# Kernel optimization log

Hardware: AMD Instinct MI355X
Metric: run time of the kernel (lower is better)

The kernel has to match this reference:

```python
import jax, jax.numpy as jnp
import numpy as np

B, L, U = 64, 512, 7          # batch, seq_len, enc_in
H = 128                        # hidden_dim
LAYERS = 2                     # num LSTM layers
PRED = 96                      # pred_len
EPS = 1e-5


def setup_inputs() -> dict:
    key = jax.random.key(0)
    ks = jax.random.split(key, 9)
    s = 0.05  # small param scale for numerical sanity
    return {
        "x": jax.random.normal(ks[0], (B, L, U), dtype=jnp.float32),
        "emb_W": jax.random.normal(ks[1], (H, 1), dtype=jnp.float32) * s,
        "emb_b": jax.random.normal(ks[2], (H,), dtype=jnp.float32) * s,
        "Wih": jax.random.normal(ks[3], (LAYERS, 4 * H, H), dtype=jnp.float32) * s,
        "Whh": jax.random.normal(ks[4], (LAYERS, 4 * H, H), dtype=jnp.float32) * s,
        "bih": jax.random.normal(ks[5], (LAYERS, 4 * H), dtype=jnp.float32) * s,
        "bhh": jax.random.normal(ks[6], (LAYERS, 4 * H), dtype=jnp.float32) * s,
        "fc_W": jax.random.normal(ks[7], (PRED, H), dtype=jnp.float32) * s,
        "fc_b": jax.random.normal(ks[8], (PRED,), dtype=jnp.float32) * s,
    }


def _lstm_layer(x, Wih, Whh, bih, bhh):
    """PyTorch-semantics single LSTM layer. x: [N, L, H_in] -> [N, L, H]."""
    N = x.shape[0]
    Hh = Whh.shape[1]
    # precompute input projections for all timesteps: [N, L, 4H]
    xp = jnp.einsum('nli,gi->nlg', x, Wih) + bih + bhh
    xp = jnp.swapaxes(xp, 0, 1)  # [L, N, 4H] for scan over time

    def step(carry, xt):
        h, c = carry
        gates = xt + h @ Whh.T           # [N, 4H]
        i, f, g, o = jnp.split(gates, 4, axis=-1)  # torch gate order i,f,g,o
        i = jax.nn.sigmoid(i)
        f = jax.nn.sigmoid(f)
        g = jnp.tanh(g)
        o = jax.nn.sigmoid(o)
        c = f * c + i * g
        h = o * jnp.tanh(c)
        return (h, c), h

    h0 = jnp.zeros((N, Hh), x.dtype)
    (_, _), hs = jax.lax.scan(step, (h0, h0), xp)
    return jnp.swapaxes(hs, 0, 1)  # [N, L, H]


def reference(x, emb_W, emb_b, Wih, Whh, bih, bhh, fc_W, fc_b):
    Bn, Ln, Un = x.shape
    # per-channel instance norm over time (stats detached in original)
    means = jax.lax.stop_gradient(jnp.mean(x, axis=1, keepdims=True))          # [B,1,U]
    stdev = jax.lax.stop_gradient(jnp.sqrt(jnp.var(x, axis=1, keepdims=True) + EPS))
    xn = (x - means) / stdev
    # NOTE: original does a raw row-major reshape (no channel permute); replicate exactly.
    xs = xn.reshape(Bn * Un, Ln, 1)                                            # [B*U, L, 1]
    h = xs @ emb_W.T + emb_b                                                   # [B*U, L, H]
    for l in range(Wih.shape[0]):
        h = _lstm_layer(h, Wih[l], Whh[l], bih[l], bhh[l])
    out = h[:, -1, :] @ fc_W.T + fc_b                                          # [B*U, PRED]
    out = out.reshape(Bn, -1, Un)                                              # [B, PRED, U]
    return out * stdev + means
```

## Files before the change

kernel.cpp:

```cpp
#include <hip/hip_runtime.h>
#include <stdint.h>

typedef short bf16x8 __attribute__((ext_vector_type(8)));
typedef float f32x4  __attribute__((ext_vector_type(4)));

#define HH 128
#define NN 448
#define PREDN 96

#define OFF_MEAN 0
#define OFF_STD  448
#define OFF_A    896
#define OFF_B0   1408
#define OFF_B1   1920
#define OFF_H1   2432
#define OFF_XSB  59776
#define OFF_WPK  174464

#define L2E  1.442695041f
#define L2E2 2.885390082f

#define ROWB 592
#define BUFB 9472

__device__ __forceinline__ float bflo(uint32_t w){ union{uint32_t u; float f;} v; v.u = w<<16; return v.f; }
__device__ __forceinline__ float bfhi(uint32_t w){ union{uint32_t u; float f;} v; v.u = w & 0xffff0000u; return v.f; }

static __device__ __forceinline__ uint32_t packbf2(float a, float b){
    union { float f; uint32_t u; } ua, ub; ua.f = a; ub.f = b;
    uint32_t x = ua.u, y = ub.u;
    uint32_t lo = (x + 0x7fffu + ((x>>16)&1u)) >> 16;
    uint32_t hi = (y + 0x7fffu + ((y>>16)&1u)) >> 16;
    return (lo & 0xffffu) | (hi<<16);
}
static __device__ __forceinline__ uint16_t bfr(float f){
    union { float f; uint32_t u; } v; v.f = f;
    return (uint16_t)((v.u + 0x7fffu + ((v.u>>16)&1u)) >> 16);
}

#if __has_builtin(__builtin_amdgcn_exp2f)
#define EXP2(x) __builtin_amdgcn_exp2f(x)
#else
#define EXP2(x) __expf(0.69314718056f*(x))
#endif
#if __has_builtin(__builtin_amdgcn_rcpf)
#define RCPF(x) __builtin_amdgcn_rcpf(x)
#else
#define RCPF(x) (1.0f/(x))
#endif

__device__ __forceinline__ float sig2(float x){ return RCPF(1.f + EXP2(-x)); }
__device__ __forceinline__ float tanh2(float xs){ return fmaf(-2.f, RCPF(EXP2(xs) + 1.f), 1.f); }

__global__ void stats_k(const float* __restrict__ x, float* __restrict__ ws){
    int bu = blockIdx.x;
    int b = bu / 7, u = bu % 7;
    int i = threadIdx.x;
    const float* p = x + b*3584 + u;
    float s = 0.f, q = 0.f;
    #pragma unroll
    for (int m=0;m<8;m++){ float v = p[(i + 64*m)*7]; s += v; q += v*v; }
    for (int o=32;o>0;o>>=1){ s += __shfl_down(s,o); q += __shfl_down(q,o); }
    if (i==0){
        float mean = s * (1.f/512.f);
        float var  = q * (1.f/512.f) - mean*mean;
        ws[OFF_MEAN + bu] = mean;
        ws[OFF_STD  + bu] = sqrtf(var + 1e-5f);
    }
}

__global__ void norm_k(const float* __restrict__ x, float* __restrict__ ws){
    int i = blockIdx.x*256 + threadIdx.x;
    int b = i / 3584, u = i % 7;
    float m = ws[OFF_MEAN + b*7 + u];
    float sd = ws[OFF_STD + b*7 + u];
    float v = (x[i] - m) / sd;
    int np = i >> 9, tp = i & 511;
    uint16_t* xb = (uint16_t*)(ws + OFF_XSB);
    xb[(np>>4)*8192 + tp*16 + (np&15)] = (uint16_t)(packbf2(v, 0.f) & 0xffffu);
}

__global__ void prep_k(const float* __restrict__ Wih, const float* __restrict__ embW,
                       const float* __restrict__ embb, const float* __restrict__ bih,
                       const float* __restrict__ bhh, float* __restrict__ ws){
    int g = threadIdx.x;
    const float* wr = Wih + g*HH;
    float a = 0.f, bb = 0.f;
    #pragma unroll 4
    for (int k=0;k<HH;k++){ a += wr[k]*embW[k]; bb += wr[k]*embb[k]; }
    ws[OFF_A  + g] = a;
    ws[OFF_B0 + g] = bb + bih[g] + bhh[g];
    ws[OFF_B1 + g] = bih[512 + g] + bhh[512 + g];
}

__global__ void prep2_k(const float* __restrict__ Whh, const float* __restrict__ Wih,
                        float* __restrict__ ws){
    int idx = blockIdx.x*256 + threadIdx.x;
    int lane = idx & 63;
    int sg = idx >> 6;
    int wvmt = sg / 13, slot = sg % 13;
    int gp  = wvmt*16 + (lane&15);
    int type = gp & 3, unit = gp >> 2;
    int row = type*128 + unit;
    float S = (type==2) ? L2E2 : L2E;
    uint4 r;
    if (slot == 4){
        r.x = r.y = r.z = r.w = 0u;
        if ((lane>>4) == 0) r.x = packbf2(ws[OFF_A+row]*S, ws[OFF_B0+row]*S);
    } else {
        const float* src; int kk;
        if (slot < 4)      { src = Whh + row*128;         kk = slot;   }
        else if (slot < 9) { src = Wih + 65536 + row*128; kk = slot-5; }
        else               { src = Whh + 65536 + row*128; kk = slot-9; }
        int k0 = kk*32 + (lane>>4)*8;
        r.x = packbf2(src[k0]*S,   src[k0+1]*S);
        r.y = packbf2(src[k0+2]*S, src[k0+3]*S);
        r.z = packbf2(src[k0+4]*S, src[k0+5]*S);
        r.w = packbf2(src[k0+6]*S, src[k0+7]*S);
    }
    ((uint4*)(ws + OFF_WPK))[sg*64 + lane] = r;
}

union FragU { bf16x8 v; uint4 q; };

__device__ __forceinline__ f32x4 mm(bf16x8 a, bf16x8 b, f32x4 c){
    return __builtin_amdgcn_mfma_f32_16x16x32_bf16(a, b, c, 0, 0, 0);
}
#define LD(p) (*(const bf16x8*)(p))

__global__ __launch_bounds__(512, 2) void lstm_core(float* __restrict__ ws)
{
    __shared__ uint16_t xsT[8192];
    __shared__ __align__(16) uint16_t hbuf[BUFB];

    const int tid = threadIdx.x;
    const int wv = tid>>6, l = tid&63;
    const int r   = l & 15;
    const int q16 = (l>>4)*16;
    const int bx = blockIdx.x, n0 = bx*16;
    char* hb = (char*)hbuf;

    const uint16_t* xb = (const uint16_t*)(ws + OFF_XSB) + bx*8192;
    for (int i=tid;i<8192;i+=512) xsT[i] = xb[i];
    for (int i=tid;i<BUFB;i+=512) hbuf[i] = 0;
    __syncthreads();
    if (tid < 32){
        int bsel = tid>>4, rr = tid&15;
        *(uint16_t*)(hb + bsel*BUFB + rr*ROWB + 514) = 0x3F80;
    }
    if (tid < 16){
        *(uint16_t*)(hb + tid*ROWB + 512) = xsT[tid];
    }

    bf16x8 wL0[4][5], wI1[4][4], wH1[4][4];
    uint32_t b1pk[4][2];
    const uint4* wpk = (const uint4*)(ws + OFF_WPK);
    #pragma unroll
    for (int mt=0;mt<4;++mt){
        int base = ((wv*4+mt)*13)*64 + l;
        #pragma unroll
        for (int kk=0;kk<5;kk++){ FragU u; u.q = wpk[base + kk*64];     wL0[mt][kk]=u.v; }
        #pragma unroll
        for (int kk=0;kk<4;kk++){ FragU u; u.q = wpk[base + (5+kk)*64]; wI1[mt][kk]=u.v; }
        #pragma unroll
        for (int kk=0;kk<4;kk++){ FragU u; u.q = wpk[base + (9+kk)*64]; wH1[mt][kk]=u.v; }
        int uu = (wv*4+mt)*4 + (l>>4);
        b1pk[mt][0] = packbf2(ws[OFF_B1+uu]*L2E,      ws[OFF_B1+128+uu]*L2E);
        b1pk[mt][1] = packbf2(ws[OFF_B1+256+uu]*L2E2, ws[OFF_B1+384+uu]*L2E);
    }

    float c0[4]={0,0,0,0}, c1[4]={0,0,0,0};
    const int rbase = r*ROWB + q16;
    const int wbase = r*ROWB + wv*32 + 2*(l>>4);

    __syncthreads();

    for (int t=0;t<512;++t){
        const int co = (t&1)*BUFB;
        const int no = BUFB - co;
        const char* pc = hb + co + rbase;
        char* pw = hb + no + wbase;

        bf16x8 f0 = LD(pc+0), f1 = LD(pc+64), f2 = LD(pc+128), f3 = LD(pc+192);
        f32x4 b0={0,0,0,0}, b1={0,0,0,0}, b2={0,0,0,0}, b3={0,0,0,0};
        __builtin_amdgcn_s_setprio(1);
        b0=mm(wI1[0][0],f0,b0); b1=mm(wI1[1][0],f0,b1); b2=mm(wI1[2][0],f0,b2); b3=mm(wI1[3][0],f0,b3);
        b0=mm(wI1[0][1],f1,b0); b1=mm(wI1[1][1],f1,b1); b2=mm(wI1[2][1],f1,b2); b3=mm(wI1[3][1],f1,b3);
        b0=mm(wI1[0][2],f2,b0); b1=mm(wI1[1][2],f2,b1); b2=mm(wI1[2][2],f2,b2); b3=mm(wI1[3][2],f2,b3);
        b0=mm(wI1[0][3],f3,b0); b1=mm(wI1[1][3],f3,b1); b2=mm(wI1[2][3],f3,b2); b3=mm(wI1[3][3],f3,b3);
        bf16x8 fa = LD(pc+512);
        f32x4 a0={0,0,0,0}, a1={0,0,0,0}, a2={0,0,0,0}, a3={0,0,0,0};
        a0=mm(wL0[0][0],f0,a0); a1=mm(wL0[1][0],f0,a1); a2=mm(wL0[2][0],f0,a2); a3=mm(wL0[3][0],f0,a3);
        a0=mm(wL0[0][1],f1,a0); a1=mm(wL0[1][1],f1,a1); a2=mm(wL0[2][1],f1,a2); a3=mm(wL0[3][1],f1,a3);
        a0=mm(wL0[0][2],f2,a0); a1=mm(wL0[1][2],f2,a1); a2=mm(wL0[2][2],f2,a2); a3=mm(wL0[3][2],f2,a3);
        a0=mm(wL0[0][3],f3,a0); a1=mm(wL0[1][3],f3,a1); a2=mm(wL0[2][3],f3,a2); a3=mm(wL0[3][3],f3,a3);
        a0=mm(wL0[0][4],fa,a0); a1=mm(wL0[1][4],fa,a1); a2=mm(wL0[2][4],fa,a2); a3=mm(wL0[3][4],fa,a3);
        __builtin_amdgcn_s_setprio(0);

        #pragma unroll
        for (int mt=0;mt<4;++mt){
            f32x4 a = (mt==0)?a0:(mt==1)?a1:(mt==2)?a2:a3;
            float i_ = sig2(a[0]);
            float f_ = sig2(a[1]);
            float g_ = tanh2(a[2]);
            float o_ = sig2(a[3]);
            float cn = fmaf(f_, c0[mt], i_*g_);
            c0[mt] = cn;
            float h = o_ * tanh2(cn*L2E2);
            *(uint16_t*)(pw + 8*mt) = bfr(h);
        }

        __builtin_amdgcn_sched_barrier(0);
        bf16x8 v0 = LD(pc+256), v1 = LD(pc+320), v2 = LD(pc+384), v3 = LD(pc+448);
        __builtin_amdgcn_s_setprio(1);
        b0=mm(wH1[0][0],v0,b0); b1=mm(wH1[1][0],v0,b1); b2=mm(wH1[2][0],v0,b2); b3=mm(wH1[3][0],v0,b3);
        b0=mm(wH1[0][1],v1,b0); b1=mm(wH1[1][1],v1,b1); b2=mm(wH1[2][1],v1,b2); b3=mm(wH1[3][1],v1,b3);
        b0=mm(wH1[0][2],v2,b0); b1=mm(wH1[1][2],v2,b1); b2=mm(wH1[2][2],v2,b2); b3=mm(wH1[3][2],v2,b3);
        b0=mm(wH1[0][3],v3,b0); b1=mm(wH1[1][3],v3,b1); b2=mm(wH1[2][3],v3,b2); b3=mm(wH1[3][3],v3,b3);
        __builtin_amdgcn_s_setprio(0);

        if (t){
            #pragma unroll
            for (int mt=0;mt<4;++mt){
                f32x4 a = (mt==0)?b0:(mt==1)?b1:(mt==2)?b2:b3;
                float i_ = sig2(a[0] + bflo(b1pk[mt][0]));
                float f_ = sig2(a[1] + bfhi(b1pk[mt][0]));
                float g_ = tanh2(a[2] + bflo(b1pk[mt][1]));
                float o_ = sig2(a[3] + bfhi(b1pk[mt][1]));
                float cn = fmaf(f_, c1[mt], i_*g_);
                c1[mt] = cn;
                float h = o_ * tanh2(cn*L2E2);
                *(uint16_t*)(pw + 256 + 8*mt) = bfr(h);
            }
        }
        if (wv==0 && l<16){
            *(uint16_t*)(hb + no + l*ROWB + 512) = xsT[((t+1)&511)*16 + l];
        }
        __syncthreads();
    }

    {
        const char* pc = hb + rbase;
        bf16x8 f0 = LD(pc+0),   f1 = LD(pc+64),  f2 = LD(pc+128), f3 = LD(pc+192);
        bf16x8 v0 = LD(pc+256), v1 = LD(pc+320), v2 = LD(pc+384), v3 = LD(pc+448);
        f32x4 b0={0,0,0,0}, b1={0,0,0,0}, b2={0,0,0,0}, b3={0,0,0,0};
        b0=mm(wI1[0][0],f0,b0); b1=mm(wI1[1][0],f0,b1); b2=mm(wI1[2][0],f0,b2); b3=mm(wI1[3][0],f0,b3);
        b0=mm(wI1[0][1],f1,b0); b1=mm(wI1[1][1],f1,b1); b2=mm(wI1[2][1],f1,b2); b3=mm(wI1[3][1],f1,b3);
        b0=mm(wI1[0][2],f2,b0); b1=mm(wI1[1][2],f2,b1); b2=mm(wI1[2][2],f2,b2); b3=mm(wI1[3][2],f2,b3);
        b0=mm(wI1[0][3],f3,b0); b1=mm(wI1[1][3],f3,b1); b2=mm(wI1[2][3],f3,b2); b3=mm(wI1[3][3],f3,b3);
        b0=mm(wH1[0][0],v0,b0); b1=mm(wH1[1][0],v0,b1); b2=mm(wH1[2][0],v0,b2); b3=mm(wH1[3][0],v0,b3);
        b0=mm(wH1[0][1],v1,b0); b1=mm(wH1[1][1],v1,b1); b2=mm(wH1[2][1],v1,b2); b3=mm(wH1[3][1],v1,b3);
        b0=mm(wH1[0][2],v2,b0); b1=mm(wH1[1][2],v2,b1); b2=mm(wH1[2][2],v2,b2); b3=mm(wH1[3][2],v2,b3);
        b0=mm(wH1[0][3],v3,b0); b1=mm(wH1[1][3],v3,b1); b2=mm(wH1[2][3],v3,b2); b3=mm(wH1[3][3],v3,b3);
        #pragma unroll
        for (int mt=0;mt<4;++mt){
            f32x4 a = (mt==0)?b0:(mt==1)?b1:(mt==2)?b2:b3;
            float i_ = sig2(a[0] + bflo(b1pk[mt][0]));
            float f_ = sig2(a[1] + bfhi(b1pk[mt][0]));
            float g_ = tanh2(a[2] + bflo(b1pk[mt][1]));
            float o_ = sig2(a[3] + bfhi(b1pk[mt][1]));
            float cn = fmaf(f_, c1[mt], i_*g_);
            float h = o_ * tanh2(cn*L2E2);
            ws[OFF_H1 + (n0+r)*128 + (wv*16 + mt*4 + (l>>4))] = h;
        }
    }
}

__global__ void out_k(const float* __restrict__ fcW, const float* __restrict__ fcb,
                      const float* __restrict__ ws, float* __restrict__ out){
    __shared__ float hl[128];
    int n = blockIdx.x, tid = threadIdx.x;
    hl[tid] = ws[OFF_H1 + n*128 + tid];
    __syncthreads();
    if (tid < PREDN){
        float acc = fcb[tid];
        const float* wr = fcW + tid*128;
        #pragma unroll 4
        for (int k=0;k<128;k++) acc += wr[k]*hl[k];
        int idx = n*PREDN + tid;
        int b = idx / 672, u = idx % 7;
        out[idx] = acc * ws[OFF_STD + b*7 + u] + ws[OFF_MEAN + b*7 + u];
    }
}

extern "C" void kernel_launch(void* const* d_in, const int* in_sizes, int n_in,
                              void* d_out, int out_size, void* d_ws, size_t ws_size,
                              hipStream_t stream)
{
    const float* x    = (const float*)d_in[0];
    const float* embW = (const float*)d_in[1];
    const float* embb = (const float*)d_in[2];
    const float* Wih  = (const float*)d_in[3];
    const float* Whh  = (const float*)d_in[4];
    const float* bih  = (const float*)d_in[5];
    const float* bhh  = (const float*)d_in[6];
    const float* fcW  = (const float*)d_in[7];
    const float* fcb  = (const float*)d_in[8];
    float* ws  = (float*)d_ws;
    float* out = (float*)d_out;

    stats_k<<<448, 64, 0, stream>>>(x, ws);
    norm_k<<<896, 256, 0, stream>>>(x, ws);
    prep_k<<<1, 512, 0, stream>>>(Wih, embW, embb, bih, bhh, ws);
    prep2_k<<<104, 256, 0, stream>>>(Whh, Wih, ws);
    lstm_core<<<28, 512, 0, stream>>>(ws);
    out_k<<<NN, 128, 0, stream>>>(fcW, fcb, ws, out);
}
```

Measured before the change: 1.132 ms.

## Permute hidden-state K layout for packed stores and reorder MFMA schedule

Weight columns are permuted at pack time so each lane's four hidden outputs land contiguously, which lets each lane write one 8-byte packed store per layer instead of four scattered 2-byte stores. The per-step loop is also reordered: all LDS fragments are loaded up front and both layers' MFMAs are issued before the layer-0 and layer-1 gate math, with the setprio and sched_barrier hints removed. This cuts LDS store instructions and aims for more MFMA/VALU overlap, at the cost of higher register pressure and the loss of the explicit priority scheduling.

```diff
diff --git a/kernel.cpp b/kernel.cpp
--- a/kernel.cpp
+++ b/kernel.cpp
@@ -32,10 +32,6 @@
     uint32_t lo = (x + 0x7fffu + ((x>>16)&1u)) >> 16;
     uint32_t hi = (y + 0x7fffu + ((y>>16)&1u)) >> 16;
     return (lo & 0xffffu) | (hi<<16);
-}
-static __device__ __forceinline__ uint16_t bfr(float f){
-    union { float f; uint32_t u; } v; v.f = f;
-    return (uint16_t)((v.u + 0x7fffu + ((v.u>>16)&1u)) >> 16);
 }
 
 #if __has_builtin(__builtin_amdgcn_exp2f)
@@ -113,10 +109,17 @@
         else if (slot < 9) { src = Wih + 65536 + row*128; kk = slot-5; }
         else               { src = Whh + 65536 + row*128; kk = slot-9; }
         int k0 = kk*32 + (lane>>4)*8;
-        r.x = packbf2(src[k0]*S,   src[k0+1]*S);
-        r.y = packbf2(src[k0+2]*S, src[k0+3]*S);
-        r.z = packbf2(src[k0+4]*S, src[k0+5]*S);
-        r.w = packbf2(src[k0+6]*S, src[k0+7]*S);
+        float c[8];
+        #pragma unroll
+        for (int j=0;j<8;j++){
+            int pj = k0 + j;
+            int cj = (pj & 0x70) | ((pj & 3) << 2) | ((pj >> 2) & 3);
+            c[j] = src[cj]*S;
+        }
+        r.x = packbf2(c[0], c[1]);
+        r.y = packbf2(c[2], c[3]);
+        r.z = packbf2(c[4], c[5]);
+        r.w = packbf2(c[6], c[7]);
     }
     ((uint4*)(ws + OFF_WPK))[sg*64 + lane] = r;
 }
@@ -136,7 +139,7 @@
     const int tid = threadIdx.x;
     const int wv = tid>>6, l = tid&63;
     const int r   = l & 15;
-    const int q16 = (l>>4)*16;
+    const int q   = l >> 4;
     const int bx = blockIdx.x, n0 = bx*16;
     char* hb = (char*)hbuf;
 
@@ -164,14 +167,14 @@
         for (int kk=0;kk<4;kk++){ FragU u; u.q = wpk[base + (5+kk)*64]; wI1[mt][kk]=u.v; }
         #pragma unroll
         for (int kk=0;kk<4;kk++){ FragU u; u.q = wpk[base + (9+kk)*64]; wH1[mt][kk]=u.v; }
-        int uu = (wv*4+mt)*4 + (l>>4);
+        int uu = (wv*4+mt)*4 + q;
         b1pk[mt][0] = packbf2(ws[OFF_B1+uu]*L2E,      ws[OFF_B1+128+uu]*L2E);
         b1pk[mt][1] = packbf2(ws[OFF_B1+256+uu]*L2E2, ws[OFF_B1+384+uu]*L2E);
     }
 
     float c0[4]={0,0,0,0}, c1[4]={0,0,0,0};
-    const int rbase = r*ROWB + q16;
-    const int wbase = r*ROWB + wv*32 + 2*(l>>4);
+    const int rbase = r*ROWB + q*16;
+    const int wbase = r*ROWB + wv*32 + q*8;
 
     __syncthreads();
 
@@ -181,45 +184,46 @@
         const char* pc = hb + co + rbase;
         char* pw = hb + no + wbase;
 
-        bf16x8 f0 = LD(pc+0), f1 = LD(pc+64), f2 = LD(pc+128), f3 = LD(pc+192);
-        f32x4 b0={0,0,0,0}, b1={0,0,0,0}, b2={0,0,0,0}, b3={0,0,0,0};
-        __builtin_amdgcn_s_setprio(1);
-        b0=mm(wI1[0][0],f0,b0); b1=mm(wI1[1][0],f0,b1); b2=mm(wI1[2][0],f0,b2); b3=mm(wI1[3][0],f0,b3);
-        b0=mm(wI1[0][1],f1,b0); b1=mm(wI1[1][1],f1,b1); b2=mm(wI1[2][1],f1,b2); b3=mm(wI1[3][1],f1,b3);
-        b0=mm(wI1[0][2],f2,b0); b1=mm(wI1[1][2],f2,b1); b2=mm(wI1[2][2],f2,b2); b3=mm(wI1[3][2],f2,b3);
-        b0=mm(wI1[0][3],f3,b0); b1=mm(wI1[1][3],f3,b1); b2=mm(wI1[2][3],f3,b2); b3=mm(wI1[3][3],f3,b3);
+        bf16x8 f0 = LD(pc+0),   f1 = LD(pc+64),  f2 = LD(pc+128), f3 = LD(pc+192);
         bf16x8 fa = LD(pc+512);
+        bf16x8 v0 = LD(pc+256), v1 = LD(pc+320), v2 = LD(pc+384), v3 = LD(pc+448);
+
         f32x4 a0={0,0,0,0}, a1={0,0,0,0}, a2={0,0,0,0}, a3={0,0,0,0};
         a0=mm(wL0[0][0],f0,a0); a1=mm(wL0[1][0],f0,a1); a2=mm(wL0[2][0],f0,a2); a3=mm(wL0[3][0],f0,a3);
         a0=mm(wL0[0][1],f1,a0); a1=mm(wL0[1][1],f1,a1); a2=mm(wL0[2][1],f1,a2); a3=mm(wL0[3][1],f1,a3);
         a0=mm(wL0[0][2],f2,a0); a1=mm(wL0[1][2],f2,a1); a2=mm(wL0[2][2],f2,a2); a3=mm(wL0[3][2],f2,a3);
         a0=mm(wL0[0][3],f3,a0); a1=mm(wL0[1][3],f3,a1); a2=mm(wL0[2][3],f3,a2); a3=mm(wL0[3][3],f3,a3);
         a0=mm(wL0[0][4],fa,a0); a1=mm(wL0[1][4],fa,a1); a2=mm(wL0[2][4],fa,a2); a3=mm(wL0[3][4],fa,a3);
-        __builtin_amdgcn_s_setprio(0);
-
-        #pragma unroll
-        for (int mt=0;mt<4;++mt){
-            f32x4 a = (mt==0)?a0:(mt==1)?a1:(mt==2)?a2:a3;
-            float i_ = sig2(a[0]);
-            float f_ = sig2(a[1]);
-            float g_ = tanh2(a[2]);
-            float o_ = sig2(a[3]);
-            float cn = fmaf(f_, c0[mt], i_*g_);
-            c0[mt] = cn;
-            float h = o_ * tanh2(cn*L2E2);
-            *(uint16_t*)(pw + 8*mt) = bfr(h);
-        }
-
-        __builtin_amdgcn_sched_barrier(0);
-        bf16x8 v0 = LD(pc+256), v1 = LD(pc+320), v2 = LD(pc+384), v3 = LD(pc+448);
-        __builtin_amdgcn_s_setprio(1);
+
+        f32x4 b0={0,0,0,0}, b1={0,0,0,0}, b2={0,0,0,0}, b3={0,0,0,0};
+        b0=mm(wI1[0][0],f0,b0); b1=mm(wI1[1][0],f0,b1); b2=mm(wI1[2][0],f0,b2); b3=mm(wI1[3][0],f0,b3);
+        b0=mm(wI1[0][1],f1,b0); b1=mm(wI1[1][1],f1,b1); b2=mm(wI1[2][1],f1,b2); b3=mm(wI1[3][1],f1,b3);
+        b0=mm(wI1[0][2],f2,b0); b1=mm(wI1[1][2],f2,b1); b2=mm(wI1[2][2],f2,b2); b3=mm(wI1[3][2],f2,b3);
+        b0=mm(wI1[0][3],f3,b0); b1=mm(wI1[1][3],f3,b1); b2=mm(wI1[2][3],f3,b2); b3=mm(wI1[3][3],f3,b3);
         b0=mm(wH1[0][0],v0,b0); b1=mm(wH1[1][0],v0,b1); b2=mm(wH1[2][0],v0,b2); b3=mm(wH1[3][0],v0,b3);
         b0=mm(wH1[0][1],v1,b0); b1=mm(wH1[1][1],v1,b1); b2=mm(wH1[2][1],v1,b2); b3=mm(wH1[3][1],v1,b3);
         b0=mm(wH1[0][2],v2,b0); b1=mm(wH1[1][2],v2,b1); b2=mm(wH1[2][2],v2,b2); b3=mm(wH1[3][2],v2,b3);
         b0=mm(wH1[0][3],v3,b0); b1=mm(wH1[1][3],v3,b1); b2=mm(wH1[2][3],v3,b2); b3=mm(wH1[3][3],v3,b3);
-        __builtin_amdgcn_s_setprio(0);
+
+        {
+            float hv[4];
+            #pragma unroll
+            for (int mt=0;mt<4;++mt){
+                f32x4 a = (mt==0)?a0:(mt==1)?a1:(mt==2)?a2:a3;
+                float i_ = sig2(a[0]);
+                float f_ = sig2(a[1]);
+                float g_ = tanh2(a[2]);
+                float o_ = sig2(a[3]);
+                float cn = fmaf(f_, c0[mt], i_*g_);
+                c0[mt] = cn;
+                hv[mt] = o_ * tanh2(cn*L2E2);
+            }
+            uint2 wq; wq.x = packbf2(hv[0],hv[1]); wq.y = packbf2(hv[2],hv[3]);
+            *(uint2*)(pw) = wq;
+        }
 
         if (t){
+            float hv[4];
             #pragma unroll
             for (int mt=0;mt<4;++mt){
                 f32x4 a = (mt==0)?b0:(mt==1)?b1:(mt==2)?b2:b3;
@@ -229,9 +233,10 @@
                 float o_ = sig2(a[3] + bfhi(b1pk[mt][1]));
                 float cn = fmaf(f_, c1[mt], i_*g_);
                 c1[mt] = cn;
-                float h = o_ * tanh2(cn*L2E2);
-                *(uint16_t*)(pw + 256 + 8*mt) = bfr(h);
+                hv[mt] = o_ * tanh2(cn*L2E2);
             }
+            uint2 wq; wq.x = packbf2(hv[0],hv[1]); wq.y = packbf2(hv[2],hv[3]);
+            *(uint2*)(pw + 256) = wq;
         }
         if (wv==0 && l<16){
             *(uint16_t*)(hb + no + l*ROWB + 512) = xsT[((t+1)&511)*16 + l];
@@ -261,7 +266,7 @@
             float o_ = sig2(a[3] + bfhi(b1pk[mt][1]));
             float cn = fmaf(f_, c1[mt], i_*g_);
             float h = o_ * tanh2(cn*L2E2);
-            ws[OFF_H1 + (n0+r)*128 + (wv*16 + mt*4 + (l>>4))] = h;
+            ws[OFF_H1 + (n0+r)*128 + (wv*16 + mt*4 + q)] = h;
         }
     }
 }
```

Measured after the change: 1.331 ms. +17.7%, slower.
